# Kernel optimization log

Hardware: AMD Instinct MI355X
Metric: run time of the kernel (lower is better)

The kernel has to match this reference:

```python
import jax, jax.numpy as jnp
import numpy as np

B, T, I = 64, 256, 768   # batch, seq_len (sentences), input_dim
H = 384                  # hidden per direction (hidden_dim // 2)
D = 768                  # hidden_dim (bidirectional concat)


def _gru_dir(x_tbi, w_ih, w_hh, b_ih, b_hh, reverse):
    """Single-direction GRU, PyTorch gate order [r, z, n]. x_tbi: [T,B,in]."""
    gx = jnp.einsum('tbi,gi->tbg', x_tbi, w_ih) + b_ih  # [T,B,3H] input gates

    def step(h, g):
        gh = h @ w_hh.T + b_hh                       # [B,3H]
        r = jax.nn.sigmoid(g[..., :H] + gh[..., :H])
        z = jax.nn.sigmoid(g[..., H:2 * H] + gh[..., H:2 * H])
        n = jnp.tanh(g[..., 2 * H:] + r * gh[..., 2 * H:])
        h_new = (1.0 - z) * n + z * h
        return h_new, h_new

    h0 = jnp.zeros((x_tbi.shape[1], H), x_tbi.dtype)
    _, ys = jax.lax.scan(step, h0, gx, reverse=reverse)  # ys in time order
    return ys


def setup_inputs() -> dict:
    key = jax.random.key(0)
    ks = jax.random.split(key, 24)
    s = 0.05
    inp = {"Sentences": jax.random.normal(ks[0], (B, T, I), dtype=jnp.float32)}
    idx = 1
    for l, in_dim in ((0, I), (1, D)):
        for d in ("f", "b"):
            inp[f"w_ih_l{l}{d}"] = jax.random.normal(ks[idx], (3 * H, in_dim), dtype=jnp.float32) * s; idx += 1
            inp[f"w_hh_l{l}{d}"] = jax.random.normal(ks[idx], (3 * H, H), dtype=jnp.float32) * s; idx += 1
            inp[f"b_ih_l{l}{d}"] = jax.random.normal(ks[idx], (3 * H,), dtype=jnp.float32) * s; idx += 1
            inp[f"b_hh_l{l}{d}"] = jax.random.normal(ks[idx], (3 * H,), dtype=jnp.float32) * s; idx += 1
    inp["fc_w"] = jax.random.normal(ks[idx], (D, D), dtype=jnp.float32) * s; idx += 1
    inp["fc_b"] = jax.random.normal(ks[idx], (D,), dtype=jnp.float32) * s; idx += 1
    inp["upw_w"] = jax.random.normal(ks[idx], (1, D), dtype=jnp.float32) * s; idx += 1
    inp["upw_b"] = jax.random.normal(ks[idx], (1,), dtype=jnp.float32) * s
    return inp


def reference(Sentences,
              w_ih_l0f, w_hh_l0f, b_ih_l0f, b_hh_l0f,
              w_ih_l0b, w_hh_l0b, b_ih_l0b, b_hh_l0b,
              w_ih_l1f, w_hh_l1f, b_ih_l1f, b_hh_l1f,
              w_ih_l1b, w_hh_l1b, b_ih_l1b, b_hh_l1b,
              fc_w, fc_b, upw_w, upw_b):
    x = jnp.transpose(Sentences, (1, 0, 2))  # [T,B,I]
    # layer 0, bidirectional
    hf = _gru_dir(x, w_ih_l0f, w_hh_l0f, b_ih_l0f, b_hh_l0f, reverse=False)
    hb = _gru_dir(x, w_ih_l0b, w_hh_l0b, b_ih_l0b, b_hh_l0b, reverse=True)
    x = jnp.concatenate([hf, hb], axis=-1)  # [T,B,D]
    # layer 1, bidirectional
    hf = _gru_dir(x, w_ih_l1f, w_hh_l1f, b_ih_l1f, b_hh_l1f, reverse=False)
    hb = _gru_dir(x, w_ih_l1b, w_hh_l1b, b_ih_l1b, b_hh_l1b, reverse=True)
    hidden = jnp.transpose(jnp.concatenate([hf, hb], axis=-1), (1, 0, 2))  # [B,T,D]
    # additive attention pooling
    u = jnp.tanh(hidden @ fc_w.T + fc_b)            # [B,T,D]
    logits = u @ upw_w.T + upw_b                    # [B,T,1]
    alpha = jax.nn.softmax(logits, axis=1)          # softmax over sentences
    return jnp.sum(alpha * hidden, axis=-2)         # [B,D]
```

## Files before the change

kernel.cpp:

```cpp
#include <hip/hip_runtime.h>

#define BB   64
#define TT   256
#define II   768
#define HH   384
#define DD   768
#define G3   1152
#define G6   2304

#define TILE 128
#define BK   16

typedef unsigned long long u64t;

__global__ __launch_bounds__(256) void gemm_gx(
    const float* __restrict__ X, int xmode,
    const float* __restrict__ wf, const float* __restrict__ wb,
    const float* __restrict__ bif, const float* __restrict__ bib,
    float* __restrict__ gx)
{
    __shared__ float As[BK][TILE + 4];
    __shared__ float Bs[BK][TILE + 4];
    const int tid = threadIdx.x;
    const int tx = tid & 15, ty = tid >> 4;
    const int m0 = blockIdx.y * TILE;
    const int n0 = blockIdx.x * TILE;

    float acc[8][8];
#pragma unroll
    for (int i = 0; i < 8; i++)
#pragma unroll
        for (int j = 0; j < 8; j++) acc[i][j] = 0.f;

    for (int k0 = 0; k0 < 768; k0 += BK) {
#pragma unroll
        for (int l = 0; l < 2; l++) {
            int id = tid + l * 256;
            int r  = id >> 2;
            int kq = (id & 3) * 4;
            int m  = m0 + r;
            const float* src;
            if (xmode == 0) {
                int b = m & 63, t = m >> 6;
                src = X + (size_t)b * (TT * II) + (size_t)t * II + k0 + kq;
            } else {
                src = X + (size_t)m * 768 + k0 + kq;
            }
            float4 v = *(const float4*)src;
            As[kq + 0][r] = v.x; As[kq + 1][r] = v.y;
            As[kq + 2][r] = v.z; As[kq + 3][r] = v.w;
        }
#pragma unroll
        for (int l = 0; l < 2; l++) {
            int id = tid + l * 256;
            int r  = id >> 2;
            int kq = (id & 3) * 4;
            int n  = n0 + r;
            const float* wsrc = (n < G3) ? (wf + (size_t)n * 768)
                                         : (wb + (size_t)(n - G3) * 768);
            float4 v = *(const float4*)(wsrc + k0 + kq);
            Bs[kq + 0][r] = v.x; Bs[kq + 1][r] = v.y;
            Bs[kq + 2][r] = v.z; Bs[kq + 3][r] = v.w;
        }
        __syncthreads();
#pragma unroll
        for (int kk = 0; kk < BK; ++kk) {
            float av[8], bv[8];
            *(float4*)&av[0] = *(const float4*)&As[kk][ty * 8];
            *(float4*)&av[4] = *(const float4*)&As[kk][ty * 8 + 4];
            *(float4*)&bv[0] = *(const float4*)&Bs[kk][tx * 8];
            *(float4*)&bv[4] = *(const float4*)&Bs[kk][tx * 8 + 4];
#pragma unroll
            for (int i = 0; i < 8; i++)
#pragma unroll
                for (int j = 0; j < 8; j++)
                    acc[i][j] = fmaf(av[i], bv[j], acc[i][j]);
        }
        __syncthreads();
    }

#pragma unroll
    for (int i = 0; i < 8; i++) {
        int m = m0 + ty * 8 + i;
        int t = m >> 6, b = m & 63;
        float* dst = gx + ((size_t)t * G6 + n0 + tx * 8) * 64 + b;
#pragma unroll
        for (int j = 0; j < 8; j++) {
            int n = n0 + tx * 8 + j;
            float bias = (n < G3) ? bif[n] : bib[n - G3];
            dst[(size_t)j * 64] = acc[i][j] + bias;
        }
    }
}

__global__ __launch_bounds__(256) void recur10(
    const float* __restrict__ gxT,
    const float* __restrict__ whf, const float* __restrict__ whb,
    const float* __restrict__ bhf, const float* __restrict__ bhb,
    unsigned* __restrict__ hv,
    float* __restrict__ out)
{
    __shared__ float part[2][4][12][64];

    const int bid  = blockIdx.x;
    const int dir  = bid / 96;
    const int c0   = (bid % 96) * 4;
    const int tid  = threadIdx.x;
    const int lane = tid & 63;
    const int w    = __builtin_amdgcn_readfirstlane(tid >> 6);
    const int c    = c0 + w;

    const float* wh = dir ? whb : whf;
    const float* bh = dir ? bhb : bhf;

    const float* wp[12];
#pragma unroll
    for (int cc = 0; cc < 4; cc++)
#pragma unroll
        for (int g = 0; g < 3; g++)
            wp[cc * 3 + g] = wh + (size_t)(g * HH + c0 + cc) * HH + w * 96;

    const float bhr = bh[c], bhz = bh[HH + c], bhn = bh[2 * HH + c];

    float hprev = 0.f;

#pragma unroll 1
    for (int s = 0; s < TT; ++s) {
        const int t  = dir ? (TT - 1 - s) : s;
        const int pp = s & 1, pn = pp ^ 1;
        const u64t* hr  = (const u64t*)hv + (size_t)(dir * 2 + pp) * 12288;
        unsigned*   hwN = hv + (size_t)(dir * 2 + pn) * 24576;
        const unsigned want8 = (unsigned)s & 0xFFu;
        const unsigned tagp  = (unsigned)(s + 1) & 0xFFu;

        const float* gA = gxT + ((size_t)t * G6 + dir * G3) * 64 + lane;
        float gr = gA[(size_t)(0 * HH + c) * 64];
        float gz = gA[(size_t)(1 * HH + c) * 64];
        float gn = gA[(size_t)(2 * HH + c) * 64];

        float acc[12];
#pragma unroll
        for (int i = 0; i < 12; i++) acc[i] = 0.f;

#pragma unroll 1
        for (int blk = 0; blk < 2; ++blk) {
            const size_t base = (size_t)(w * 48 + blk * 24) * 64 + lane;
            u64t v[24];
            while (true) {
#pragma unroll
                for (int j = 0; j < 24; ++j)
                    v[j] = __hip_atomic_load(hr + base + (size_t)j * 64,
                                             __ATOMIC_RELAXED,
                                             __HIP_MEMORY_SCOPE_AGENT);
                bool ok = true;
#pragma unroll
                for (int j = 0; j < 24; ++j)
                    ok = ok && (((unsigned)v[j] & 0xFFu) == want8)
                            && (((unsigned)(v[j] >> 32) & 0xFFu) == want8);
                if (__all(ok)) break;
                __builtin_amdgcn_s_sleep(1);
            }
#pragma unroll
            for (int j = 0; j < 24; ++j) {
                float h0 = __uint_as_float((unsigned)v[j]);
                float h1 = __uint_as_float((unsigned)(v[j] >> 32));
                const int ko = blk * 48 + j * 2;
#pragma unroll
                for (int cg = 0; cg < 12; ++cg) {
                    acc[cg] = fmaf(h0, wp[cg][ko],     acc[cg]);
                    acc[cg] = fmaf(h1, wp[cg][ko + 1], acc[cg]);
                }
            }
        }

#pragma unroll
        for (int cg = 0; cg < 12; ++cg)
            part[pp][w][cg][lane] = acc[cg];
        __syncthreads();

        const int d0 = w * 3;
        float ar = part[pp][0][d0 + 0][lane] + part[pp][1][d0 + 0][lane]
                 + part[pp][2][d0 + 0][lane] + part[pp][3][d0 + 0][lane];
        float az = part[pp][0][d0 + 1][lane] + part[pp][1][d0 + 1][lane]
                 + part[pp][2][d0 + 1][lane] + part[pp][3][d0 + 1][lane];
        float an = part[pp][0][d0 + 2][lane] + part[pp][1][d0 + 2][lane]
                 + part[pp][2][d0 + 2][lane] + part[pp][3][d0 + 2][lane];

        float ghr = ar + bhr, ghz = az + bhz, ghn = an + bhn;
        float rr  = 1.f / (1.f + expf(-(gr + ghr)));
        float zz  = 1.f / (1.f + expf(-(gz + ghz)));
        float nn  = tanhf(gn + rr * ghn);
        float hnew = (1.f - zz) * nn + zz * hprev;
        hprev = hnew;

        unsigned bits = (__float_as_uint(hnew) & 0xFFFFFF00u) | tagp;
        __hip_atomic_store(hwN + (size_t)(c >> 1) * 128 + lane * 2 + (c & 1),
                           bits, __ATOMIC_RELAXED, __HIP_MEMORY_SCOPE_AGENT);
        out[(size_t)t * (BB * DD) + (size_t)lane * DD + dir * HH + c] = hnew;
    }
}

__global__ __launch_bounds__(256) void attn_logits(
    const float* __restrict__ Xh,
    const float* __restrict__ fcw,
    const float* __restrict__ fcb, const float* __restrict__ upw,
    float* __restrict__ logits)
{
    __shared__ float As[BK][TILE + 4];
    __shared__ float Bs[BK][TILE + 4];
    __shared__ float red[TILE][17];
    const int tid = threadIdx.x;
    const int tx = tid & 15, ty = tid >> 4;
    const int m0 = blockIdx.y * TILE;
    const int n0 = blockIdx.x * TILE;

    float acc[8][8];
#pragma unroll
    for (int i = 0; i < 8; i++)
#pragma unroll
        for (int j = 0; j < 8; j++) acc[i][j] = 0.f;

    for (int k0 = 0; k0 < 768; k0 += BK) {
#pragma unroll
        for (int l = 0; l < 2; l++) {
            int id = tid + l * 256;
            int r  = id >> 2;
            int kq = (id & 3) * 4;
            float4 v = *(const float4*)(Xh + (size_t)(m0 + r) * 768 + k0 + kq);
            As[kq + 0][r] = v.x; As[kq + 1][r] = v.y;
            As[kq + 2][r] = v.z; As[kq + 3][r] = v.w;
        }
#pragma unroll
        for (int l = 0; l < 2; l++) {
            int id = tid + l * 256;
            int r  = id >> 2;
            int kq = (id & 3) * 4;
            float4 v = *(const float4*)(fcw + (size_t)(n0 + r) * 768 + k0 + kq);
            Bs[kq + 0][r] = v.x; Bs[kq + 1][r] = v.y;
            Bs[kq + 2][r] = v.z; Bs[kq + 3][r] = v.w;
        }
        __syncthreads();
#pragma unroll
        for (int kk = 0; kk < BK; ++kk) {
            float av[8], bv[8];
            *(float4*)&av[0] = *(const float4*)&As[kk][ty * 8];
            *(float4*)&av[4] = *(const float4*)&As[kk][ty * 8 + 4];
            *(float4*)&bv[0] = *(const float4*)&Bs[kk][tx * 8];
            *(float4*)&bv[4] = *(const float4*)&Bs[kk][tx * 8 + 4];
#pragma unroll
            for (int i = 0; i < 8; i++)
#pragma unroll
                for (int j = 0; j < 8; j++)
                    acc[i][j] = fmaf(av[i], bv[j], acc[i][j]);
        }
        __syncthreads();
    }

#pragma unroll
    for (int i = 0; i < 8; i++) {
        float p = 0.f;
#pragma unroll
        for (int jj = 0; jj < 8; jj++) {
            int n = n0 + tx * 8 + jj;
            p += tanhf(acc[i][jj] + fcb[n]) * upw[n];
        }
        red[ty * 8 + i][tx] = p;
    }
    __syncthreads();
    if (tid < TILE) {
        float s = 0.f;
#pragma unroll
        for (int xk = 0; xk < 16; xk++) s += red[tid][xk];
        int m = m0 + tid;
        int t = m >> 6, b = m & 63;
        atomicAdd(&logits[(size_t)b * TT + t], s);
    }
}

__global__ __launch_bounds__(256) void softmax_pool(
    const float* __restrict__ logits, const float* __restrict__ upwb,
    const float* __restrict__ hidden, float* __restrict__ out)
{
    const int b = blockIdx.x, tid = threadIdx.x;
    __shared__ float sa[256];
    __shared__ float red[256];

    float l = logits[(size_t)b * TT + tid] + upwb[0];
    red[tid] = l; __syncthreads();
    for (int s = 128; s > 0; s >>= 1) {
        if (tid < s) red[tid] = fmaxf(red[tid], red[tid + s]);
        __syncthreads();
    }
    float mx = red[0];
    __syncthreads();
    float e = expf(l - mx);
    sa[tid] = e; red[tid] = e; __syncthreads();
    for (int s = 128; s > 0; s >>= 1) {
        if (tid < s) red[tid] += red[tid + s];
        __syncthreads();
    }
    float inv = 1.f / red[0];

    float o0 = 0.f, o1 = 0.f, o2 = 0.f;
    for (int t = 0; t < TT; t++) {
        float a = sa[t] * inv;
        const float* hp = hidden + (size_t)t * (BB * DD) + (size_t)b * DD;
        o0 = fmaf(a, hp[tid],       o0);
        o1 = fmaf(a, hp[tid + 256], o1);
        o2 = fmaf(a, hp[tid + 512], o2);
    }
    out[(size_t)b * DD + tid]       = o0;
    out[(size_t)b * DD + tid + 256] = o1;
    out[(size_t)b * DD + tid + 512] = o2;
}

extern "C" void kernel_launch(void* const* d_in, const int* in_sizes, int n_in,
                              void* d_out, int out_size, void* d_ws, size_t ws_size,
                              hipStream_t stream)
{
    const float* S        = (const float*)d_in[0];
    const float* w_ih_l0f = (const float*)d_in[1];
    const float* w_hh_l0f = (const float*)d_in[2];
    const float* b_ih_l0f = (const float*)d_in[3];
    const float* b_hh_l0f = (const float*)d_in[4];
    const float* w_ih_l0b = (const float*)d_in[5];
    const float* w_hh_l0b = (const float*)d_in[6];
    const float* b_ih_l0b = (const float*)d_in[7];
    const float* b_hh_l0b = (const float*)d_in[8];
    const float* w_ih_l1f = (const float*)d_in[9];
    const float* w_hh_l1f = (const float*)d_in[10];
    const float* b_ih_l1f = (const float*)d_in[11];
    const float* b_hh_l1f = (const float*)d_in[12];
    const float* w_ih_l1b = (const float*)d_in[13];
    const float* w_hh_l1b = (const float*)d_in[14];
    const float* b_ih_l1b = (const float*)d_in[15];
    const float* b_hh_l1b = (const float*)d_in[16];
    const float* fc_w     = (const float*)d_in[17];
    const float* fc_b     = (const float*)d_in[18];
    const float* upw_w    = (const float*)d_in[19];
    const float* upw_b    = (const float*)d_in[20];

    float* gxT     = (float*)d_ws;
    float* buf2    = gxT  + (size_t)TT * G6 * BB;
    unsigned* hv0  = (unsigned*)(buf2 + (size_t)TT * BB * DD);
    unsigned* hv1  = hv0 + 98304;
    float* logits  = (float*)(hv1 + 98304);

    hipMemsetAsync(hv0, 0, (size_t)(2 * 98304 + 16384) * 4, stream);

    gemm_gx<<<dim3(18, 128), 256, 0, stream>>>(S, 0, w_ih_l0f, w_ih_l0b,
                                               b_ih_l0f, b_ih_l0b, gxT);
    {
        void* args[] = {(void*)&gxT, (void*)&w_hh_l0f, (void*)&w_hh_l0b,
                        (void*)&b_hh_l0f, (void*)&b_hh_l0b, (void*)&hv0,
                        (void*)&buf2};
        hipLaunchCooperativeKernel((const void*)recur10, dim3(192), dim3(256),
                                   args, 0, stream);
    }
    gemm_gx<<<dim3(18, 128), 256, 0, stream>>>(buf2, 1, w_ih_l1f, w_ih_l1b,
                                               b_ih_l1f, b_ih_l1b, gxT);
    {
        void* args[] = {(void*)&gxT, (void*)&w_hh_l1f, (void*)&w_hh_l1b,
                        (void*)&b_hh_l1f, (void*)&b_hh_l1b, (void*)&hv1,
                        (void*)&buf2};
        hipLaunchCooperativeKernel((const void*)recur10, dim3(192), dim3(256),
                                   args, 0, stream);
    }
    attn_logits<<<dim3(6, 128), 256, 0, stream>>>(buf2, fc_w, fc_b, upw_w, logits);
    softmax_pool<<<64, 256, 0, stream>>>(logits, upw_b, buf2, (float*)d_out);
}
```

Measured before the change: 7.340 ms.

## Split GRU recurrence by batch groups with LDS-resident weights and local flag buffers

Replaces the cooperative recurrence kernel with a version where 256 blocks each own an 8-batch group, one direction and a 24-column slice. Each block caches its W_hh slice in LDS, reads the tagged hidden state with wide asm vector loads, and reduces over k with wavefront shuffles instead of an LDS cross-wave reduction and __syncthreads. Hidden-state publication is duplicated into a near-cache buffer and an agent-scope buffer, with a fallback to the coherent one after repeated spin failures. The gx layout is changed to batch-grouped rows to match. This targets per-step global weight traffic and synchronisation latency, at the cost of a large LDS footprint, more blocks spinning, and reliance on cache-bypass semantics for correctness.

```diff
diff --git a/kernel.cpp b/kernel.cpp
--- a/kernel.cpp
+++ b/kernel.cpp
@@ -12,6 +12,7 @@
 #define BK   16
 
 typedef unsigned long long u64t;
+typedef __attribute__((ext_vector_type(4))) float f32x4;
 
 __global__ __launch_bounds__(256) void gemm_gx(
     const float* __restrict__ X, int xmode,
@@ -83,120 +84,172 @@
     for (int i = 0; i < 8; i++) {
         int m = m0 + ty * 8 + i;
         int t = m >> 6, b = m & 63;
-        float* dst = gx + ((size_t)t * G6 + n0 + tx * 8) * 64 + b;
+        int bg = b >> 3, b8 = b & 7;
+        float* dst = gx + (((size_t)t * 8 + bg) * G6 + n0 + tx * 8) * 8 + b8;
 #pragma unroll
         for (int j = 0; j < 8; j++) {
             int n = n0 + tx * 8 + j;
             float bias = (n < G3) ? bif[n] : bib[n - G3];
-            dst[(size_t)j * 64] = acc[i][j] + bias;
+            dst[(size_t)j * 8] = acc[i][j] + bias;
         }
     }
 }
 
-__global__ __launch_bounds__(256) void recur10(
+
+#define HLOAD(SCB) \
+    asm volatile( \
+        "global_load_dwordx4 %0,  %12, off " SCB "\n\t" \
+        "global_load_dwordx4 %1,  %12, off offset:16 " SCB "\n\t" \
+        "global_load_dwordx4 %2,  %12, off offset:32 " SCB "\n\t" \
+        "global_load_dwordx4 %3,  %12, off offset:48 " SCB "\n\t" \
+        "global_load_dwordx4 %4,  %12, off offset:64 " SCB "\n\t" \
+        "global_load_dwordx4 %5,  %12, off offset:80 " SCB "\n\t" \
+        "global_load_dwordx4 %6,  %12, off offset:96 " SCB "\n\t" \
+        "global_load_dwordx4 %7,  %12, off offset:112 " SCB "\n\t" \
+        "global_load_dwordx4 %8,  %12, off offset:128 " SCB "\n\t" \
+        "global_load_dwordx4 %9,  %12, off offset:144 " SCB "\n\t" \
+        "global_load_dwordx4 %10, %12, off offset:160 " SCB "\n\t" \
+        "global_load_dwordx4 %11, %12, off offset:176 " SCB "\n\t" \
+        "s_waitcnt vmcnt(0)" \
+        : "=&v"(F[0]), "=&v"(F[1]), "=&v"(F[2]),  "=&v"(F[3]), \
+          "=&v"(F[4]), "=&v"(F[5]), "=&v"(F[6]),  "=&v"(F[7]), \
+          "=&v"(F[8]), "=&v"(F[9]), "=&v"(F[10]), "=&v"(F[11]) \
+        : "v"(hb) : "memory")
+
+__global__ __launch_bounds__(256) void recur11(
     const float* __restrict__ gxT,
     const float* __restrict__ whf, const float* __restrict__ whb,
     const float* __restrict__ bhf, const float* __restrict__ bhb,
-    unsigned* __restrict__ hv,
+    unsigned* __restrict__ hl,
+    unsigned* __restrict__ hm,
     float* __restrict__ out)
 {
-    __shared__ float part[2][4][12][64];
+    extern __shared__ float wlds[];
 
     const int bid  = blockIdx.x;
-    const int dir  = bid / 96;
-    const int c0   = (bid % 96) * 4;
+    const int x    = bid & 7;
+    const int j    = bid >> 3;
+    const int dir  = j & 1;
+    const int c0   = (j >> 1) * 24;
     const int tid  = threadIdx.x;
+    const int w    = __builtin_amdgcn_readfirstlane(tid >> 6);
     const int lane = tid & 63;
-    const int w    = __builtin_amdgcn_readfirstlane(tid >> 6);
-    const int c    = c0 + w;
+    const int b    = lane >> 3;
+    const int ks   = lane & 7;
+    const int c0w  = c0 + w * 6;
 
     const float* wh = dir ? whb : whf;
     const float* bh = dir ? bhb : bhf;
 
-    const float* wp[12];
-#pragma unroll
-    for (int cc = 0; cc < 4; cc++)
-#pragma unroll
-        for (int g = 0; g < 3; g++)
-            wp[cc * 3 + g] = wh + (size_t)(g * HH + c0 + cc) * HH + w * 96;
-
-    const float bhr = bh[c], bhz = bh[HH + c], bhn = bh[2 * HH + c];
-
-    float hprev = 0.f;
+    for (int i = tid; i < 72 * 96; i += 256) {
+        int row = i / 96;
+        int kq  = (i % 96) * 4;
+        int cc = row / 3, g = row % 3;
+        float4 v = *(const float4*)(wh + (size_t)(g * HH + c0 + cc) * HH + kq);
+        *(float4*)&wlds[row * 416 + (kq / 48) * 52 + (kq % 48)] = v;
+    }
+    __syncthreads();
+
+    float bR[6], bZ[6], bN[6];
+#pragma unroll
+    for (int q = 0; q < 6; q++) {
+        bR[q] = bh[c0w + q];
+        bZ[q] = bh[HH + c0w + q];
+        bN[q] = bh[2 * HH + c0w + q];
+    }
+
+    unsigned* hlx = hl + ((size_t)x * 2 + dir) * 6144;
+    unsigned* hmx = hm + ((size_t)x * 2 + dir) * 6144;
+
+    float hprev[6] = {0.f, 0.f, 0.f, 0.f, 0.f, 0.f};
+    bool uloc = true;
 
 #pragma unroll 1
     for (int s = 0; s < TT; ++s) {
         const int t  = dir ? (TT - 1 - s) : s;
         const int pp = s & 1, pn = pp ^ 1;
-        const u64t* hr  = (const u64t*)hv + (size_t)(dir * 2 + pp) * 12288;
-        unsigned*   hwN = hv + (size_t)(dir * 2 + pn) * 24576;
         const unsigned want8 = (unsigned)s & 0xFFu;
         const unsigned tagp  = (unsigned)(s + 1) & 0xFFu;
 
-        const float* gA = gxT + ((size_t)t * G6 + dir * G3) * 64 + lane;
-        float gr = gA[(size_t)(0 * HH + c) * 64];
-        float gz = gA[(size_t)(1 * HH + c) * 64];
-        float gn = gA[(size_t)(2 * HH + c) * 64];
-
-        float acc[12];
-#pragma unroll
-        for (int i = 0; i < 12; i++) acc[i] = 0.f;
-
-#pragma unroll 1
-        for (int blk = 0; blk < 2; ++blk) {
-            const size_t base = (size_t)(w * 48 + blk * 24) * 64 + lane;
-            u64t v[24];
-            while (true) {
-#pragma unroll
-                for (int j = 0; j < 24; ++j)
-                    v[j] = __hip_atomic_load(hr + base + (size_t)j * 64,
-                                             __ATOMIC_RELAXED,
-                                             __HIP_MEMORY_SCOPE_AGENT);
-                bool ok = true;
-#pragma unroll
-                for (int j = 0; j < 24; ++j)
-                    ok = ok && (((unsigned)v[j] & 0xFFu) == want8)
-                            && (((unsigned)(v[j] >> 32) & 0xFFu) == want8);
-                if (__all(ok)) break;
-                __builtin_amdgcn_s_sleep(1);
+        float gxr[6], gxz[6], gxn[6];
+        if (ks == 0) {
+            const float* gb = gxT + (((size_t)t * 8 + x) * G6 + dir * G3) * 8 + b;
+#pragma unroll
+            for (int q = 0; q < 6; q++) {
+                int c = c0w + q;
+                gxr[q] = gb[(size_t)(0 * HH + c) * 8];
+                gxz[q] = gb[(size_t)(1 * HH + c) * 8];
+                gxn[q] = gb[(size_t)(2 * HH + c) * 8];
             }
-#pragma unroll
-            for (int j = 0; j < 24; ++j) {
-                float h0 = __uint_as_float((unsigned)v[j]);
-                float h1 = __uint_as_float((unsigned)(v[j] >> 32));
-                const int ko = blk * 48 + j * 2;
-#pragma unroll
-                for (int cg = 0; cg < 12; ++cg) {
-                    acc[cg] = fmaf(h0, wp[cg][ko],     acc[cg]);
-                    acc[cg] = fmaf(h1, wp[cg][ko + 1], acc[cg]);
-                }
+        }
+
+        const unsigned* hlb = hlx + pp * 3072 + b * 384 + ks * 48;
+        const unsigned* hmb = hmx + pp * 3072 + b * 384 + ks * 48;
+        f32x4 F[12];
+        int tries = 0;
+        for (;;) {
+            if (uloc) { const unsigned* hb = hlb; HLOAD("sc0"); }
+            else      { const unsigned* hb = hmb; HLOAD("sc0 sc1"); }
+            bool ok = true;
+#pragma unroll
+            for (int i2 = 0; i2 < 12; ++i2) {
+                ok = ok && ((__float_as_uint(F[i2].x) & 0xFFu) == want8)
+                        && ((__float_as_uint(F[i2].y) & 0xFFu) == want8)
+                        && ((__float_as_uint(F[i2].z) & 0xFFu) == want8)
+                        && ((__float_as_uint(F[i2].w) & 0xFFu) == want8);
             }
-        }
-
-#pragma unroll
-        for (int cg = 0; cg < 12; ++cg)
-            part[pp][w][cg][lane] = acc[cg];
-        __syncthreads();
-
-        const int d0 = w * 3;
-        float ar = part[pp][0][d0 + 0][lane] + part[pp][1][d0 + 0][lane]
-                 + part[pp][2][d0 + 0][lane] + part[pp][3][d0 + 0][lane];
-        float az = part[pp][0][d0 + 1][lane] + part[pp][1][d0 + 1][lane]
-                 + part[pp][2][d0 + 1][lane] + part[pp][3][d0 + 1][lane];
-        float an = part[pp][0][d0 + 2][lane] + part[pp][1][d0 + 2][lane]
-                 + part[pp][2][d0 + 2][lane] + part[pp][3][d0 + 2][lane];
-
-        float ghr = ar + bhr, ghz = az + bhz, ghn = an + bhn;
-        float rr  = 1.f / (1.f + expf(-(gr + ghr)));
-        float zz  = 1.f / (1.f + expf(-(gz + ghz)));
-        float nn  = tanhf(gn + rr * ghn);
-        float hnew = (1.f - zz) * nn + zz * hprev;
-        hprev = hnew;
-
-        unsigned bits = (__float_as_uint(hnew) & 0xFFFFFF00u) | tagp;
-        __hip_atomic_store(hwN + (size_t)(c >> 1) * 128 + lane * 2 + (c & 1),
-                           bits, __ATOMIC_RELAXED, __HIP_MEMORY_SCOPE_AGENT);
-        out[(size_t)t * (BB * DD) + (size_t)lane * DD + dir * HH + c] = hnew;
+            if (__all(ok)) break;
+            if (uloc && (++tries > 200)) uloc = false;
+            __builtin_amdgcn_s_sleep(1);
+        }
+
+        float acc[18];
+#pragma unroll
+        for (int r = 0; r < 18; ++r) acc[r] = 0.f;
+#pragma unroll
+        for (int kk = 0; kk < 12; ++kk) {
+            f32x4 hv = F[kk];
+#pragma unroll
+            for (int r = 0; r < 18; ++r) {
+                const f32x4 wv =
+                    *(const f32x4*)&wlds[(w * 18 + r) * 416 + ks * 52 + kk * 4];
+                acc[r] = fmaf(hv.x, wv.x, acc[r]);
+                acc[r] = fmaf(hv.y, wv.y, acc[r]);
+                acc[r] = fmaf(hv.z, wv.z, acc[r]);
+                acc[r] = fmaf(hv.w, wv.w, acc[r]);
+            }
+        }
+
+#pragma unroll
+        for (int r = 0; r < 18; ++r) {
+            acc[r] += __shfl_down(acc[r], 4);
+            acc[r] += __shfl_down(acc[r], 2);
+            acc[r] += __shfl_down(acc[r], 1);
+        }
+
+        if (ks == 0) {
+            unsigned* hlp = hlx + pn * 3072 + b * 384;
+            unsigned* hmp = hmx + pn * 3072 + b * 384;
+            float*    op  = out + ((size_t)t * BB + x * 8 + b) * DD + dir * HH;
+#pragma unroll
+            for (int q = 0; q < 6; ++q) {
+                float ghr = acc[q * 3 + 0] + bR[q];
+                float ghz = acc[q * 3 + 1] + bZ[q];
+                float ghn = acc[q * 3 + 2] + bN[q];
+                float rr = 1.f / (1.f + expf(-(gxr[q] + ghr)));
+                float zz = 1.f / (1.f + expf(-(gxz[q] + ghz)));
+                float nn = tanhf(gxn[q] + rr * ghn);
+                float hnew = (1.f - zz) * nn + zz * hprev[q];
+                hprev[q] = hnew;
+
+                unsigned bits = (__float_as_uint(hnew) & 0xFFFFFF00u) | tagp;
+                __hip_atomic_store(hlp + c0w + q, bits, __ATOMIC_RELAXED,
+                                   __HIP_MEMORY_SCOPE_WORKGROUP);
+                __hip_atomic_store(hmp + c0w + q, bits, __ATOMIC_RELAXED,
+                                   __HIP_MEMORY_SCOPE_AGENT);
+                op[c0w + q] = hnew;
+            }
+        }
     }
 }
 
@@ -342,29 +395,33 @@
 
     float* gxT     = (float*)d_ws;
     float* buf2    = gxT  + (size_t)TT * G6 * BB;
-    unsigned* hv0  = (unsigned*)(buf2 + (size_t)TT * BB * DD);
-    unsigned* hv1  = hv0 + 98304;
-    float* logits  = (float*)(hv1 + 98304);
-
-    hipMemsetAsync(hv0, 0, (size_t)(2 * 98304 + 16384) * 4, stream);
+    unsigned* hl0  = (unsigned*)(buf2 + (size_t)TT * BB * DD);
+    unsigned* hm0  = hl0 + 98304;
+    unsigned* hl1  = hm0 + 98304;
+    unsigned* hm1  = hl1 + 98304;
+    float* logits  = (float*)(hm1 + 98304);
+
+    const size_t LDSZ = 72 * 416 * sizeof(float);
+
+    hipMemsetAsync(hl0, 0, (size_t)(4 * 98304 + 16384) * 4, stream);
 
     gemm_gx<<<dim3(18, 128), 256, 0, stream>>>(S, 0, w_ih_l0f, w_ih_l0b,
                                                b_ih_l0f, b_ih_l0b, gxT);
     {
         void* args[] = {(void*)&gxT, (void*)&w_hh_l0f, (void*)&w_hh_l0b,
-                        (void*)&b_hh_l0f, (void*)&b_hh_l0b, (void*)&hv0,
-                        (void*)&buf2};
-        hipLaunchCooperativeKernel((const void*)recur10, dim3(192), dim3(256),
-                                   args, 0, stream);
+                        (void*)&b_hh_l0f, (void*)&b_hh_l0b, (void*)&hl0,
+                        (void*)&hm0, (void*)&buf2};
+        hipLaunchCooperativeKernel((const void*)recur11, dim3(256), dim3(256),
+                                   args, LDSZ, stream);
     }
     gemm_gx<<<dim3(18, 128), 256, 0, stream>>>(buf2, 1, w_ih_l1f, w_ih_l1b,
                                                b_ih_l1f, b_ih_l1b, gxT);
     {
         void* args[] = {(void*)&gxT, (void*)&w_hh_l1f, (void*)&w_hh_l1b,
-                        (void*)&b_hh_l1f, (void*)&b_hh_l1b, (void*)&hv1,
-                        (void*)&buf2};
-        hipLaunchCooperativeKernel((const void*)recur10, dim3(192), dim3(256),
-                                   args, 0, stream);
+                        (void*)&b_hh_l1f, (void*)&b_hh_l1b, (void*)&hl1,
+                        (void*)&hm1, (void*)&buf2};
+        hipLaunchCooperativeKernel((const void*)recur11, dim3(256), dim3(256),
+                                   args, LDSZ, stream);
     }
     attn_logits<<<dim3(6, 128), 256, 0, stream>>>(buf2, fc_w, fc_b, upw_w, logits);
     softmax_pool<<<64, 256, 0, stream>>>(logits, upw_b, buf2, (float*)d_out);
```

After: 23.70 ms. +223.0%, slower.
